# Performance work log

Hardware: AMD Instinct MI355X
Metric: run time of the kernel (lower is better)

Reference implementation:

```python
import jax, jax.numpy as jnp
import numpy as np

S, E = 4, 8                      # num_species, ensemble size
DIMS = [384, 160, 128, 96, 1]    # AEV dim -> hidden dims -> energy
ALPHA = 0.1                      # CELU alpha (ANI default)
N_ATOMS = 100000


def setup_inputs() -> dict:
    key = jax.random.key(0)
    k_aev, k_sp = jax.random.split(key, 2)
    aev = jax.random.normal(k_aev, (N_ATOMS, DIMS[0]), dtype=jnp.float32)
    species = jax.random.randint(k_sp, (N_ATOMS,), 0, S)
    inp = {"aev": aev, "species": species}
    for l in range(4):
        kw = jax.random.fold_in(key, 10 + l)
        kb = jax.random.fold_in(key, 20 + l)
        scale = 1.0 / np.float32(np.sqrt(DIMS[l]))
        inp[f"W{l+1}"] = jax.random.normal(kw, (S, E, DIMS[l], DIMS[l + 1]), dtype=jnp.float32) * scale
        inp[f"b{l+1}"] = jax.random.normal(kb, (S, E, 1, DIMS[l + 1]), dtype=jnp.float32) * 0.01
    return inp


def _forward(aev, species, W1, b1, W2, b2, W3, b3, W4, b4):
    # Faithful math: E_total = sum_a mean_e( net_{species[a]}^{(e)}(aev[a]) )
    # Original gathers rows per species (dynamic shapes); for jit-compatibility we run
    # each species' ensemble net over all atoms and mask the per-atom outputs before
    # the scatter-sum. Per-atom results are identical.
    Ws = [W1, W2, W3, W4]
    bs = [b1, b2, b3, b4]
    total = jnp.zeros((), dtype=aev.dtype)
    for s in range(S):  # small fixed species count
        # BmmLinear: baddbmm over ensemble dim e
        x = jnp.einsum('ni,eio->eno', aev, Ws[0][s]) + bs[0][s]  # [E, N, h1]
        for l in range(1, 4):
            x = jax.nn.celu(x, ALPHA)
            x = jnp.einsum('eni,eio->eno', x, Ws[l][s]) + bs[l][s]
        out = x.mean(axis=0)[:, 0]  # mean over ensemble -> [N]
        total = total + jnp.sum(jnp.where(species == s, out, jnp.zeros((), out.dtype)))
    return total[None]  # torch.sum(energy_list, 0, True) -> shape [1]


def reference(aev, species, W1, b1, W2, b2, W3, b3, W4, b4):
    return _forward(aev, species, W1, b1, W2, b2, W3, b3, W4, b4)
```

## Files before the change

kernel.cpp:

```cpp
#include <hip/hip_runtime.h>
#include <stdint.h>

#define N_ATOMS 100000
#define NS 4
#define NE 8
#define D0 384
#define D1 160
#define D2 128
#define D3 96
#define TW 32
#define BUCKET_CAP 32768

#define IDX_OFF_B 256
#define IDX_CAP (NS*BUCKET_CAP)
#define W1B_OFF (IDX_OFF_B + IDX_CAP*4)
#define W1_TOT (NS*NE*D0*D1)
#define W2_TOT (NS*NE*D1*D2)
#define W3_TOT (NS*NE*D2*D3)
#define W2B_OFF (W1B_OFF + W1_TOT*2)
#define W3B_OFF (W2B_OFF + W2_TOT*2)

#define S1STR 172
#define S2STR 140

#define P1TILES 3072
#define P1BLOCKS 768
#define MAXTILES 3128
#define TAILBLOCKS 112
#define GRID_MLP (P1BLOCKS + TAILBLOCKS)

typedef __attribute__((ext_vector_type(8))) _Float16 h8v;
typedef __attribute__((ext_vector_type(4))) float f4v;

__device__ __forceinline__ unsigned short f2h(float x){
    _Float16 h = (_Float16)x;
    return *(unsigned short*)&h;
}

__device__ __forceinline__ float celu01(float v){
    return v > 0.f ? v : 0.1f * (__expf(fminf(v, 0.f) * 10.f) - 1.f);
}

__global__ void k_init(int* hdr, float* out){
    int i = threadIdx.x;
    if (i < 32) hdr[i] = 0;
    if (i == 0) out[0] = 0.f;
}

__global__ __launch_bounds__(256) void k_scatter(const int* __restrict__ species,
                                                 int* __restrict__ hdr,
                                                 int* __restrict__ idx){
    __shared__ int lc[NS];
    __shared__ int lb[NS];
    int tid = threadIdx.x;
    if (tid < NS) lc[tid] = 0;
    __syncthreads();
    int i = blockIdx.x * 256 + tid;
    int s = 0, r = 0;
    bool valid = (i < N_ATOMS);
    if (valid){
        s = species[i];
        r = atomicAdd(&lc[s], 1);
    }
    __syncthreads();
    if (tid < NS) lb[tid] = atomicAdd(&hdr[tid], lc[tid]);
    __syncthreads();
    if (valid) idx[s * BUCKET_CAP + lb[s] + r] = i;
}

__global__ void k_scan(int* hdr){
    int tb = 0;
    hdr[16] = 0;
    for (int s = 0; s < 4; s++){
        int tiles = (hdr[s] + TW - 1) / TW;
        tb += tiles;
        hdr[17 + s] = tb;
    }
}

__global__ void k_convert(const float* __restrict__ W1, const float* __restrict__ W2,
                          const float* __restrict__ W3,
                          unsigned short* __restrict__ W1b, unsigned short* __restrict__ W2b,
                          unsigned short* __restrict__ W3b){
    int i = blockIdx.x * blockDim.x + threadIdx.x;
    if (i < W1_TOT){
        int net = i / (D0*D1);
        int r   = i % (D0*D1);
        int j = r & 7, lane = (r >> 3) & 63, kt = (r >> 9) % 12, nt = r / 6144;
        int k = kt*32 + (lane >> 4)*8 + j;
        int n = nt*16 + (lane & 15);
        W1b[i] = f2h(W1[(net*D0 + k)*D1 + n]);
    } else if (i < W1_TOT + W2_TOT){
        int i2 = i - W1_TOT;
        int net = i2 / (D1*D2);
        int r   = i2 % (D1*D2);
        int j = r & 7, lane = (r >> 3) & 63, kt = (r >> 9) % 5, nt = r / 2560;
        int k = kt*32 + (lane >> 4)*8 + j;
        int n = nt*16 + (lane & 15);
        W2b[i2] = f2h(W2[(net*D1 + k)*D2 + n]);
    } else if (i < W1_TOT + W2_TOT + W3_TOT){
        int i3 = i - W1_TOT - W2_TOT;
        int net = i3 / (D2*D3);
        int r   = i3 % (D2*D3);
        int j = r & 7, lane = (r >> 3) & 63, kt = (r >> 9) % 4, nt = r / 2048;
        int k = kt*32 + (lane >> 4)*8 + j;
        int n = nt*16 + (lane & 15);
        W3b[i3] = f2h(W3[(net*D2 + k)*D3 + n]);
    }
}

__global__ __launch_bounds__(256, 2) void k_mlp(
    const float* __restrict__ aev, const int* __restrict__ hdr, const int* __restrict__ idx,
    const unsigned short* __restrict__ W1b, const unsigned short* __restrict__ W2b,
    const unsigned short* __restrict__ W3b,
    const float* __restrict__ b1, const float* __restrict__ b2, const float* __restrict__ b3,
    const float* __restrict__ W4, const float* __restrict__ b4, float* __restrict__ out)
{
    __shared__ __align__(16) unsigned short sBuf[4][TW*S1STR];

    int tid = threadIdx.x;
    int lane = tid & 63, wid = tid >> 6;
    int total = hdr[20];
    int bi = blockIdx.x;
    int tileId, eBeg, eEnd;
    if (bi < P1BLOCKS){
        tileId = (bi & 7) * (P1TILES/8) + (bi >> 3) * 4 + wid;
        eBeg = 0; eEnd = NE;
    } else {
        int u = (bi - P1BLOCKS) * 4 + wid;
        tileId = P1TILES + (u >> 3);
        eBeg = u & 7; eEnd = eBeg + 1;
    }
    if (tileId >= total) return;

    int s = 0;
    while (s < 3 && tileId >= hdr[17 + s]) s++;
    int t       = tileId - hdr[16 + s];
    int count   = hdr[s];
    int rowBase = t * TW;
    const int* myIdx = idx + s * BUCKET_CAP + rowBase;
    int nValid = count - rowBase; if (nValid > TW) nValid = TW;

    int m = lane & 15, quad = lane >> 4;
    unsigned short (*X1)[S1STR] = (unsigned short (*)[S1STR])sBuf[wid];
    unsigned short (*X2)[S2STR] = (unsigned short (*)[S2STR])sBuf[wid];

    h8v A1[2][12];
    #pragma unroll
    for (int mt = 0; mt < 2; mt++){
        int slot = mt*16 + m;
        int atom = myIdx[(slot < nValid) ? slot : 0];
        const float* ap = aev + (size_t)atom * D0 + quad*8;
        #pragma unroll
        for (int kt = 0; kt < 12; kt++){
            float4 u = *(const float4*)(ap + kt*32);
            float4 v = *(const float4*)(ap + kt*32 + 4);
            h8v f;
            f[0] = (_Float16)u.x; f[1] = (_Float16)u.y; f[2] = (_Float16)u.z; f[3] = (_Float16)u.w;
            f[4] = (_Float16)v.x; f[5] = (_Float16)v.y; f[6] = (_Float16)v.z; f[7] = (_Float16)v.w;
            A1[mt][kt] = f;
        }
    }

    float e0[4] = {0.f,0.f,0.f,0.f};
    float e1[4] = {0.f,0.f,0.f,0.f};

    #pragma unroll 1
    for (int e = eBeg; e < eEnd; e++){
        int net = s * NE + e;

        {
            const unsigned short* wf = W1b + (size_t)net * (D0*D1) + lane*8;
            h8v Bb[2][12];
            #pragma unroll
            for (int kt = 0; kt < 12; kt++) Bb[0][kt] = *(const h8v*)(wf + kt*512);
            #pragma unroll
            for (int nt = 0; nt < 10; nt++){
                int cur = nt & 1, nxt = cur ^ 1;
                if (nt < 9){
                    const unsigned short* bp = wf + (nt+1)*6144;
                    #pragma unroll
                    for (int kt = 0; kt < 12; kt++) Bb[nxt][kt] = *(const h8v*)(bp + kt*512);
                }
                float bi1 = b1[net*D1 + nt*16 + m];
                f4v a0e = {bi1, bi1, bi1, bi1}, a1e = a0e;
                f4v a0o = {0.f,0.f,0.f,0.f}, a1o = a0o;
                #pragma unroll
                for (int kt = 0; kt < 12; kt += 2){
                    a0e = __builtin_amdgcn_mfma_f32_16x16x32_f16(A1[0][kt],   Bb[cur][kt],   a0e, 0, 0, 0);
                    a1e = __builtin_amdgcn_mfma_f32_16x16x32_f16(A1[1][kt],   Bb[cur][kt],   a1e, 0, 0, 0);
                    a0o = __builtin_amdgcn_mfma_f32_16x16x32_f16(A1[0][kt+1], Bb[cur][kt+1], a0o, 0, 0, 0);
                    a1o = __builtin_amdgcn_mfma_f32_16x16x32_f16(A1[1][kt+1], Bb[cur][kt+1], a1o, 0, 0, 0);
                }
                f4v a0 = a0e + a0o, a1 = a1e + a1o;
                #pragma unroll
                for (int r = 0; r < 4; r++){
                    X1[quad*4 + r][nt*16 + m]      = f2h(celu01(a0[r]));
                    X1[16 + quad*4 + r][nt*16 + m] = f2h(celu01(a1[r]));
                }
            }
        }

        {
            h8v A2[2][5];
            #pragma unroll
            for (int mt = 0; mt < 2; mt++)
                #pragma unroll
                for (int kt = 0; kt < 5; kt++)
                    A2[mt][kt] = *(const h8v*)&X1[mt*16 + m][kt*32 + quad*8];
            const unsigned short* wf = W2b + (size_t)net * (D1*D2) + lane*8;
            h8v Bb[2][5];
            #pragma unroll
            for (int kt = 0; kt < 5; kt++) Bb[0][kt] = *(const h8v*)(wf + kt*512);
            #pragma unroll
            for (int nt = 0; nt < 8; nt++){
                int cur = nt & 1, nxt = cur ^ 1;
                if (nt < 7){
                    const unsigned short* bp = wf + (nt+1)*2560;
                    #pragma unroll
                    for (int kt = 0; kt < 5; kt++) Bb[nxt][kt] = *(const h8v*)(bp + kt*512);
                }
                float bi2 = b2[net*D2 + nt*16 + m];
                f4v a0e = {bi2, bi2, bi2, bi2}, a1e = a0e;
                f4v a0o = {0.f,0.f,0.f,0.f}, a1o = a0o;
                #pragma unroll
                for (int kt = 0; kt < 5; kt++){
                    if ((kt & 1) == 0){
                        a0e = __builtin_amdgcn_mfma_f32_16x16x32_f16(A2[0][kt], Bb[cur][kt], a0e, 0, 0, 0);
                        a1e = __builtin_amdgcn_mfma_f32_16x16x32_f16(A2[1][kt], Bb[cur][kt], a1e, 0, 0, 0);
                    } else {
                        a0o = __builtin_amdgcn_mfma_f32_16x16x32_f16(A2[0][kt], Bb[cur][kt], a0o, 0, 0, 0);
                        a1o = __builtin_amdgcn_mfma_f32_16x16x32_f16(A2[1][kt], Bb[cur][kt], a1o, 0, 0, 0);
                    }
                }
                f4v a0 = a0e + a0o, a1 = a1e + a1o;
                #pragma unroll
                for (int r = 0; r < 4; r++){
                    X2[quad*4 + r][nt*16 + m]      = f2h(celu01(a0[r]));
                    X2[16 + quad*4 + r][nt*16 + m] = f2h(celu01(a1[r]));
                }
            }
        }

        {
            h8v A3[2][4];
            #pragma unroll
            for (int mt = 0; mt < 2; mt++)
                #pragma unroll
                for (int kt = 0; kt < 4; kt++)
                    A3[mt][kt] = *(const h8v*)&X2[mt*16 + m][kt*32 + quad*8];
            const unsigned short* wf = W3b + (size_t)net * (D2*D3) + lane*8;
            const float* w4 = W4 + net * D3;
            h8v Bb[2][4];
            #pragma unroll
            for (int kt = 0; kt < 4; kt++) Bb[0][kt] = *(const h8v*)(wf + kt*512);
            #pragma unroll
            for (int nt = 0; nt < 6; nt++){
                int cur = nt & 1, nxt = cur ^ 1;
                if (nt < 5){
                    const unsigned short* bp = wf + (nt+1)*2048;
                    #pragma unroll
                    for (int kt = 0; kt < 4; kt++) Bb[nxt][kt] = *(const h8v*)(bp + kt*512);
                }
                float bi3 = b3[net*D3 + nt*16 + m];
                f4v a0e = {bi3, bi3, bi3, bi3}, a1e = a0e;
                f4v a0o = {0.f,0.f,0.f,0.f}, a1o = a0o;
                #pragma unroll
                for (int kt = 0; kt < 4; kt += 2){
                    a0e = __builtin_amdgcn_mfma_f32_16x16x32_f16(A3[0][kt],   Bb[cur][kt],   a0e, 0, 0, 0);
                    a1e = __builtin_amdgcn_mfma_f32_16x16x32_f16(A3[1][kt],   Bb[cur][kt],   a1e, 0, 0, 0);
                    a0o = __builtin_amdgcn_mfma_f32_16x16x32_f16(A3[0][kt+1], Bb[cur][kt+1], a0o, 0, 0, 0);
                    a1o = __builtin_amdgcn_mfma_f32_16x16x32_f16(A3[1][kt+1], Bb[cur][kt+1], a1o, 0, 0, 0);
                }
                f4v a0 = a0e + a0o, a1 = a1e + a1o;
                float w = w4[nt*16 + m];
                #pragma unroll
                for (int r = 0; r < 4; r++){
                    e0[r] = fmaf(celu01(a0[r]), w, e0[r]);
                    e1[r] = fmaf(celu01(a1[r]), w, e1[r]);
                }
            }
        }
    }

    {
        float tot = 0.f;
        #pragma unroll
        for (int r = 0; r < 4; r++){
            tot += (quad*4 + r      < nValid) ? e0[r] : 0.f;
            tot += (16 + quad*4 + r < nValid) ? e1[r] : 0.f;
        }
        tot += __shfl_xor(tot, 1, 64);
        tot += __shfl_xor(tot, 2, 64);
        tot += __shfl_xor(tot, 4, 64);
        tot += __shfl_xor(tot, 8, 64);
        tot += __shfl_xor(tot, 16, 64);
        tot += __shfl_xor(tot, 32, 64);
        if (lane == 0){
            float sb4 = 0.f;
            for (int e = eBeg; e < eEnd; e++) sb4 += b4[s*NE + e];
            atomicAdd(out, (tot + (float)nValid * sb4) * 0.125f);
        }
    }
}

extern "C" void kernel_launch(void* const* d_in, const int* in_sizes, int n_in,
                              void* d_out, int out_size, void* d_ws, size_t ws_size,
                              hipStream_t stream){
    const float* aev     = (const float*)d_in[0];
    const int*   species = (const int*)  d_in[1];
    const float* W1 = (const float*)d_in[2];
    const float* b1 = (const float*)d_in[3];
    const float* W2 = (const float*)d_in[4];
    const float* b2 = (const float*)d_in[5];
    const float* W3 = (const float*)d_in[6];
    const float* b3 = (const float*)d_in[7];
    const float* W4 = (const float*)d_in[8];
    const float* b4 = (const float*)d_in[9];
    float* out = (float*)d_out;

    int* hdr = (int*)d_ws;
    int* idx = (int*)((char*)d_ws + IDX_OFF_B);
    unsigned short* W1b = (unsigned short*)((char*)d_ws + W1B_OFF);
    unsigned short* W2b = (unsigned short*)((char*)d_ws + W2B_OFF);
    unsigned short* W3b = (unsigned short*)((char*)d_ws + W3B_OFF);

    k_init   <<<1, 64, 0, stream>>>(hdr, out);
    k_scatter<<<(N_ATOMS + 255)/256, 256, 0, stream>>>(species, hdr, idx);
    k_scan   <<<1, 1, 0, stream>>>(hdr);
    int convTot = W1_TOT + W2_TOT + W3_TOT;
    k_convert<<<(convTot + 255)/256, 256, 0, stream>>>(W1, W2, W3, W1b, W2b, W3b);
    k_mlp    <<<GRID_MLP, 256, 0, stream>>>(aev, hdr, idx, W1b, W2b, W3b,
                                            b1, b2, b3, W4, b4, out);
}
```

Baseline: 526.9 us.

## Share weight tiles across warps via LDS staging with global_load_lds double buffering

```diff
diff --git a/kernel.cpp b/kernel.cpp
--- a/kernel.cpp
+++ b/kernel.cpp
@@ -8,7 +8,6 @@
 #define D1 160
 #define D2 128
 #define D3 96
-#define TW 32
 #define BUCKET_CAP 32768
 
 #define IDX_OFF_B 256
@@ -20,17 +19,18 @@
 #define W2B_OFF (W1B_OFF + W1_TOT*2)
 #define W3B_OFF (W2B_OFF + W2_TOT*2)
 
-#define S1STR 172
-#define S2STR 140
-
-#define P1TILES 3072
 #define P1BLOCKS 768
-#define MAXTILES 3128
-#define TAILBLOCKS 112
-#define GRID_MLP (P1BLOCKS + TAILBLOCKS)
+#define GRID_MLP (P1BLOCKS + 17*4)
 
 typedef __attribute__((ext_vector_type(8))) _Float16 h8v;
 typedef __attribute__((ext_vector_type(4))) float f4v;
+
+typedef __attribute__((address_space(3))) unsigned int lds_uint;
+typedef __attribute__((address_space(1))) const unsigned int glob_uint;
+
+__device__ __forceinline__ void gll16(const unsigned short* gp, unsigned short* lp){
+    __builtin_amdgcn_global_load_lds((glob_uint*)gp, (lds_uint*)lp, 16, 0, 0);
+}
 
 __device__ __forceinline__ unsigned short f2h(float x){
     _Float16 h = (_Float16)x;
@@ -39,6 +39,10 @@
 
 __device__ __forceinline__ float celu01(float v){
     return v > 0.f ? v : 0.1f * (__expf(fminf(v, 0.f) * 10.f) - 1.f);
+}
+
+__device__ __forceinline__ int swzb(int row, int colByte, int strideB){
+    return (row * strideB + colByte) ^ ((row & 7) << 4);
 }
 
 __global__ void k_init(int* hdr, float* out){
@@ -66,16 +70,6 @@
     if (tid < NS) lb[tid] = atomicAdd(&hdr[tid], lc[tid]);
     __syncthreads();
     if (valid) idx[s * BUCKET_CAP + lb[s] + r] = i;
-}
-
-__global__ void k_scan(int* hdr){
-    int tb = 0;
-    hdr[16] = 0;
-    for (int s = 0; s < 4; s++){
-        int tiles = (hdr[s] + TW - 1) / TW;
-        tb += tiles;
-        hdr[17 + s] = tb;
-    }
 }
 
 __global__ void k_convert(const float* __restrict__ W1, const float* __restrict__ W2,
@@ -109,52 +103,56 @@
     }
 }
 
-__global__ __launch_bounds__(256, 2) void k_mlp(
+__global__ __launch_bounds__(256, 3) void k_mlp(
     const float* __restrict__ aev, const int* __restrict__ hdr, const int* __restrict__ idx,
     const unsigned short* __restrict__ W1b, const unsigned short* __restrict__ W2b,
     const unsigned short* __restrict__ W3b,
     const float* __restrict__ b1, const float* __restrict__ b2, const float* __restrict__ b3,
     const float* __restrict__ W4, const float* __restrict__ b4, float* __restrict__ out)
 {
-    __shared__ __align__(16) unsigned short sBuf[4][TW*S1STR];
+    __shared__ __align__(128) unsigned short sX[4][5120];
+    __shared__ __align__(128) unsigned short stg[2][3072];
 
     int tid = threadIdx.x;
     int lane = tid & 63, wid = tid >> 6;
-    int total = hdr[20];
-    int bi = blockIdx.x;
-    int tileId, eBeg, eEnd;
-    if (bi < P1BLOCKS){
-        tileId = (bi & 7) * (P1TILES/8) + (bi >> 3) * 4 + wid;
+
+    int c0 = hdr[0], c1 = hdr[1], c2 = hdr[2], c3 = hdr[3];
+    int n0 = (c0 + 127) >> 7, n1 = (c1 + 127) >> 7, n2 = (c2 + 127) >> 7, n3 = (c3 + 127) >> 7;
+    int p1 = n0, p2 = p1 + n1, p3 = p2 + n2, nb = p3 + n3;
+
+    int g, eBeg, eEnd;
+    if (blockIdx.x < P1BLOCKS){
+        g = (blockIdx.x & 7) * 96 + (blockIdx.x >> 3);
         eBeg = 0; eEnd = NE;
     } else {
-        int u = (bi - P1BLOCKS) * 4 + wid;
-        tileId = P1TILES + (u >> 3);
-        eBeg = u & 7; eEnd = eBeg + 1;
-    }
-    if (tileId >= total) return;
-
-    int s = 0;
-    while (s < 3 && tileId >= hdr[17 + s]) s++;
-    int t       = tileId - hdr[16 + s];
-    int count   = hdr[s];
-    int rowBase = t * TW;
-    const int* myIdx = idx + s * BUCKET_CAP + rowBase;
-    int nValid = count - rowBase; if (nValid > TW) nValid = TW;
+        int RT = nb - P1BLOCKS;
+        int u = blockIdx.x - P1BLOCKS;
+        if (u >= RT * 4) return;
+        g = P1BLOCKS + (u >> 2);
+        eBeg = (u & 3) * 2; eEnd = eBeg + 2;
+    }
+
+    int s   = (g >= p3) ? 3 : (g >= p2) ? 2 : (g >= p1) ? 1 : 0;
+    int blk = g - (s == 0 ? 0 : s == 1 ? p1 : s == 2 ? p2 : p3);
+    int cs  = (s == 0 ? c0 : s == 1 ? c1 : s == 2 ? c2 : c3);
+    int base = blk * 128 + wid * 32;
+    int nValid = cs - base; if (nValid > 32) nValid = 32; if (nValid < 0) nValid = 0;
+    const int* myIdx = idx + s * BUCKET_CAP + base;
 
     int m = lane & 15, quad = lane >> 4;
-    unsigned short (*X1)[S1STR] = (unsigned short (*)[S1STR])sBuf[wid];
-    unsigned short (*X2)[S2STR] = (unsigned short (*)[S2STR])sBuf[wid];
+    char* xb = (char*)sX[wid];
 
     h8v A1[2][12];
     #pragma unroll
     for (int mt = 0; mt < 2; mt++){
         int slot = mt*16 + m;
-        int atom = myIdx[(slot < nValid) ? slot : 0];
+        int atom = 0;
+        if (nValid > 0) atom = myIdx[slot < nValid ? slot : nValid - 1];
         const float* ap = aev + (size_t)atom * D0 + quad*8;
         #pragma unroll
         for (int kt = 0; kt < 12; kt++){
-            float4 u = *(const float4*)(ap + kt*32);
-            float4 v = *(const float4*)(ap + kt*32 + 4);
+            f4v u = __builtin_nontemporal_load((const f4v*)(ap + kt*32));
+            f4v v = __builtin_nontemporal_load((const f4v*)(ap + kt*32 + 4));
             h8v f;
             f[0] = (_Float16)u.x; f[1] = (_Float16)u.y; f[2] = (_Float16)u.z; f[3] = (_Float16)u.w;
             f[4] = (_Float16)v.x; f[5] = (_Float16)v.y; f[6] = (_Float16)v.z; f[7] = (_Float16)v.w;
@@ -165,39 +163,55 @@
     float e0[4] = {0.f,0.f,0.f,0.f};
     float e1[4] = {0.f,0.f,0.f,0.f};
 
+    #define STAGE(P, src, dst) \
+        for (int p = wid; p < (P); p += 4) gll16((src) + p*512 + lane*8, (dst) + p*512);
+
     #pragma unroll 1
     for (int e = eBeg; e < eEnd; e++){
         int net = s * NE + e;
 
         {
-            const unsigned short* wf = W1b + (size_t)net * (D0*D1) + lane*8;
-            h8v Bb[2][12];
-            #pragma unroll
-            for (int kt = 0; kt < 12; kt++) Bb[0][kt] = *(const h8v*)(wf + kt*512);
-            #pragma unroll
+            const unsigned short* w1 = W1b + (size_t)net * (D0*D1);
+            STAGE(6, w1, stg[0]);
+            __syncthreads();
+            #pragma unroll 1
             for (int nt = 0; nt < 10; nt++){
-                int cur = nt & 1, nxt = cur ^ 1;
-                if (nt < 9){
-                    const unsigned short* bp = wf + (nt+1)*6144;
-                    #pragma unroll
-                    for (int kt = 0; kt < 12; kt++) Bb[nxt][kt] = *(const h8v*)(bp + kt*512);
-                }
+                STAGE(6, w1 + (2*nt + 1)*3072, stg[1]);
                 float bi1 = b1[net*D1 + nt*16 + m];
                 f4v a0e = {bi1, bi1, bi1, bi1}, a1e = a0e;
-                f4v a0o = {0.f,0.f,0.f,0.f}, a1o = a0o;
-                #pragma unroll
-                for (int kt = 0; kt < 12; kt += 2){
-                    a0e = __builtin_amdgcn_mfma_f32_16x16x32_f16(A1[0][kt],   Bb[cur][kt],   a0e, 0, 0, 0);
-                    a1e = __builtin_amdgcn_mfma_f32_16x16x32_f16(A1[1][kt],   Bb[cur][kt],   a1e, 0, 0, 0);
-                    a0o = __builtin_amdgcn_mfma_f32_16x16x32_f16(A1[0][kt+1], Bb[cur][kt+1], a0o, 0, 0, 0);
-                    a1o = __builtin_amdgcn_mfma_f32_16x16x32_f16(A1[1][kt+1], Bb[cur][kt+1], a1o, 0, 0, 0);
+                f4v a0o = {0.f,0.f,0.f,0.f},   a1o = a0o;
+                #pragma unroll
+                for (int k2 = 0; k2 < 6; k2++){
+                    h8v B = *(const h8v*)&stg[0][k2*512 + lane*8];
+                    if ((k2 & 1) == 0){
+                        a0e = __builtin_amdgcn_mfma_f32_16x16x32_f16(A1[0][k2], B, a0e, 0, 0, 0);
+                        a1e = __builtin_amdgcn_mfma_f32_16x16x32_f16(A1[1][k2], B, a1e, 0, 0, 0);
+                    } else {
+                        a0o = __builtin_amdgcn_mfma_f32_16x16x32_f16(A1[0][k2], B, a0o, 0, 0, 0);
+                        a1o = __builtin_amdgcn_mfma_f32_16x16x32_f16(A1[1][k2], B, a1o, 0, 0, 0);
+                    }
+                }
+                __syncthreads();
+                if (nt < 9) STAGE(6, w1 + (2*nt + 2)*3072, stg[0]);
+                #pragma unroll
+                for (int k2 = 0; k2 < 6; k2++){
+                    h8v B = *(const h8v*)&stg[1][k2*512 + lane*8];
+                    if ((k2 & 1) == 0){
+                        a0e = __builtin_amdgcn_mfma_f32_16x16x32_f16(A1[0][6+k2], B, a0e, 0, 0, 0);
+                        a1e = __builtin_amdgcn_mfma_f32_16x16x32_f16(A1[1][6+k2], B, a1e, 0, 0, 0);
+                    } else {
+                        a0o = __builtin_amdgcn_mfma_f32_16x16x32_f16(A1[0][6+k2], B, a0o, 0, 0, 0);
+                        a1o = __builtin_amdgcn_mfma_f32_16x16x32_f16(A1[1][6+k2], B, a1o, 0, 0, 0);
+                    }
                 }
                 f4v a0 = a0e + a0o, a1 = a1e + a1o;
+                int colB = (nt*16 + m)*2;
                 #pragma unroll
                 for (int r = 0; r < 4; r++){
-                    X1[quad*4 + r][nt*16 + m]      = f2h(celu01(a0[r]));
-                    X1[16 + quad*4 + r][nt*16 + m] = f2h(celu01(a1[r]));
-                }
+                    *(unsigned short*)(xb + swzb(quad*4 + r,      colB, 320)) = f2h(celu01(a0[r]));
+                    *(unsigned short*)(xb + swzb(16 + quad*4 + r, colB, 320)) = f2h(celu01(a1[r]));
+                }
+                __syncthreads();
             }
         }
 
@@ -207,38 +221,36 @@
             for (int mt = 0; mt < 2; mt++)
                 #pragma unroll
                 for (int kt = 0; kt < 5; kt++)
-                    A2[mt][kt] = *(const h8v*)&X1[mt*16 + m][kt*32 + quad*8];
-            const unsigned short* wf = W2b + (size_t)net * (D1*D2) + lane*8;
-            h8v Bb[2][5];
-            #pragma unroll
-            for (int kt = 0; kt < 5; kt++) Bb[0][kt] = *(const h8v*)(wf + kt*512);
-            #pragma unroll
+                    A2[mt][kt] = *(const h8v*)(xb + swzb(mt*16 + m, (kt*32 + quad*8)*2, 320));
+            const unsigned short* w2 = W2b + (size_t)net * (D1*D2);
+            STAGE(5, w2, stg[0]);
+            __syncthreads();
+            #pragma unroll 1
             for (int nt = 0; nt < 8; nt++){
-                int cur = nt & 1, nxt = cur ^ 1;
-                if (nt < 7){
-                    const unsigned short* bp = wf + (nt+1)*2560;
-                    #pragma unroll
-                    for (int kt = 0; kt < 5; kt++) Bb[nxt][kt] = *(const h8v*)(bp + kt*512);
-                }
+                int buf = nt & 1;
+                if (nt < 7) STAGE(5, w2 + (nt + 1)*2560, stg[buf ^ 1]);
                 float bi2 = b2[net*D2 + nt*16 + m];
                 f4v a0e = {bi2, bi2, bi2, bi2}, a1e = a0e;
-                f4v a0o = {0.f,0.f,0.f,0.f}, a1o = a0o;
+                f4v a0o = {0.f,0.f,0.f,0.f},   a1o = a0o;
                 #pragma unroll
                 for (int kt = 0; kt < 5; kt++){
+                    h8v B = *(const h8v*)&stg[buf][kt*512 + lane*8];
                     if ((kt & 1) == 0){
-                        a0e = __builtin_amdgcn_mfma_f32_16x16x32_f16(A2[0][kt], Bb[cur][kt], a0e, 0, 0, 0);
-                        a1e = __builtin_amdgcn_mfma_f32_16x16x32_f16(A2[1][kt], Bb[cur][kt], a1e, 0, 0, 0);
+                        a0e = __builtin_amdgcn_mfma_f32_16x16x32_f16(A2[0][kt], B, a0e, 0, 0, 0);
+                        a1e = __builtin_amdgcn_mfma_f32_16x16x32_f16(A2[1][kt], B, a1e, 0, 0, 0);
                     } else {
-                        a0o = __builtin_amdgcn_mfma_f32_16x16x32_f16(A2[0][kt], Bb[cur][kt], a0o, 0, 0, 0);
-                        a1o = __builtin_amdgcn_mfma_f32_16x16x32_f16(A2[1][kt], Bb[cur][kt], a1o, 0, 0, 0);
+                        a0o = __builtin_amdgcn_mfma_f32_16x16x32_f16(A2[0][kt], B, a0o, 0, 0, 0);
+                        a1o = __builtin_amdgcn_mfma_f32_16x16x32_f16(A2[1][kt], B, a1o, 0, 0, 0);
                     }
                 }
                 f4v a0 = a0e + a0o, a1 = a1e + a1o;
+                int colB = (nt*16 + m)*2;
                 #pragma unroll
                 for (int r = 0; r < 4; r++){
-                    X2[quad*4 + r][nt*16 + m]      = f2h(celu01(a0[r]));
-                    X2[16 + quad*4 + r][nt*16 + m] = f2h(celu01(a1[r]));
-                }
+                    *(unsigned short*)(xb + swzb(quad*4 + r,      colB, 256)) = f2h(celu01(a0[r]));
+                    *(unsigned short*)(xb + swzb(16 + quad*4 + r, colB, 256)) = f2h(celu01(a1[r]));
+                }
+                __syncthreads();
             }
         }
 
@@ -248,29 +260,28 @@
             for (int mt = 0; mt < 2; mt++)
                 #pragma unroll
                 for (int kt = 0; kt < 4; kt++)
-                    A3[mt][kt] = *(const h8v*)&X2[mt*16 + m][kt*32 + quad*8];
-            const unsigned short* wf = W3b + (size_t)net * (D2*D3) + lane*8;
+                    A3[mt][kt] = *(const h8v*)(xb + swzb(mt*16 + m, (kt*32 + quad*8)*2, 256));
+            const unsigned short* w3 = W3b + (size_t)net * (D2*D3);
             const float* w4 = W4 + net * D3;
-            h8v Bb[2][4];
-            #pragma unroll
-            for (int kt = 0; kt < 4; kt++) Bb[0][kt] = *(const h8v*)(wf + kt*512);
-            #pragma unroll
+            STAGE(4, w3, stg[0]);
+            __syncthreads();
+            #pragma unroll 1
             for (int nt = 0; nt < 6; nt++){
-                int cur = nt & 1, nxt = cur ^ 1;
-                if (nt < 5){
-                    const unsigned short* bp = wf + (nt+1)*2048;
-                    #pragma unroll
-                    for (int kt = 0; kt < 4; kt++) Bb[nxt][kt] = *(const h8v*)(bp + kt*512);
-                }
+                int buf = nt & 1;
+                if (nt < 5) STAGE(4, w3 + (nt + 1)*2048, stg[buf ^ 1]);
                 float bi3 = b3[net*D3 + nt*16 + m];
                 f4v a0e = {bi3, bi3, bi3, bi3}, a1e = a0e;
-                f4v a0o = {0.f,0.f,0.f,0.f}, a1o = a0o;
-                #pragma unroll
-                for (int kt = 0; kt < 4; kt += 2){
-                    a0e = __builtin_amdgcn_mfma_f32_16x16x32_f16(A3[0][kt],   Bb[cur][kt],   a0e, 0, 0, 0);
-                    a1e = __builtin_amdgcn_mfma_f32_16x16x32_f16(A3[1][kt],   Bb[cur][kt],   a1e, 0, 0, 0);
-                    a0o = __builtin_amdgcn_mfma_f32_16x16x32_f16(A3[0][kt+1], Bb[cur][kt+1], a0o, 0, 0, 0);
-                    a1o = __builtin_amdgcn_mfma_f32_16x16x32_f16(A3[1][kt+1], Bb[cur][kt+1], a1o, 0, 0, 0);
+                f4v a0o = {0.f,0.f,0.f,0.f},   a1o = a0o;
+                #pragma unroll
+                for (int kt = 0; kt < 4; kt++){
+                    h8v B = *(const h8v*)&stg[buf][kt*512 + lane*8];
+                    if ((kt & 1) == 0){
+                        a0e = __builtin_amdgcn_mfma_f32_16x16x32_f16(A3[0][kt], B, a0e, 0, 0, 0);
+                        a1e = __builtin_amdgcn_mfma_f32_16x16x32_f16(A3[1][kt], B, a1e, 0, 0, 0);
+                    } else {
+                        a0o = __builtin_amdgcn_mfma_f32_16x16x32_f16(A3[0][kt], B, a0o, 0, 0, 0);
+                        a1o = __builtin_amdgcn_mfma_f32_16x16x32_f16(A3[1][kt], B, a1o, 0, 0, 0);
+                    }
                 }
                 f4v a0 = a0e + a0o, a1 = a1e + a1o;
                 float w = w4[nt*16 + m];
@@ -279,6 +290,7 @@
                     e0[r] = fmaf(celu01(a0[r]), w, e0[r]);
                     e1[r] = fmaf(celu01(a1[r]), w, e1[r]);
                 }
+                __syncthreads();
             }
         }
     }
@@ -296,12 +308,13 @@
         tot += __shfl_xor(tot, 8, 64);
         tot += __shfl_xor(tot, 16, 64);
         tot += __shfl_xor(tot, 32, 64);
-        if (lane == 0){
+        if (lane == 0 && nValid > 0){
             float sb4 = 0.f;
             for (int e = eBeg; e < eEnd; e++) sb4 += b4[s*NE + e];
             atomicAdd(out, (tot + (float)nValid * sb4) * 0.125f);
         }
     }
+    #undef STAGE
 }
 
 extern "C" void kernel_launch(void* const* d_in, const int* in_sizes, int n_in,
@@ -327,7 +340,6 @@
 
     k_init   <<<1, 64, 0, stream>>>(hdr, out);
     k_scatter<<<(N_ATOMS + 255)/256, 256, 0, stream>>>(species, hdr, idx);
-    k_scan   <<<1, 1, 0, stream>>>(hdr);
     int convTot = W1_TOT + W2_TOT + W3_TOT;
     k_convert<<<(convTot + 255)/256, 256, 0, stream>>>(W1, W2, W3, W1b, W2b, W3b);
     k_mlp    <<<GRID_MLP, 256, 0, stream>>>(aev, hdr, idx, W1b, W2b, W3b,
```

Result: slower. 611.3 us (+16.0%).
